# Kernel optimization log

Hardware: AMD Instinct MI355X
Metric: run time of the kernel (lower is better)

Reference implementation:

```python
import jax, jax.numpy as jnp
import numpy as np

N_TREES, DEPTH, INPUT_DIM, N_CLASSES = 15, 3, 128, 10
N_LEAVES = 2 ** DEPTH
N_INTERNAL = N_LEAVES - 1


def _path_masks(depth):
    """Right/left ancestor indicator matrices [n_leaves, n_internal]."""
    n_leaves = 2 ** depth
    n_int = n_leaves - 1
    R = np.zeros((n_leaves, n_int), np.float32)
    L = np.zeros((n_leaves, n_int), np.float32)
    for leaf in range(n_leaves):
        node = leaf + n_int
        for _ in range(depth):
            parent = (node - 1) // 2
            if node % 2 == 0:
                R[leaf, parent] = 1.0
            else:
                L[leaf, parent] = 1.0
            node = parent
    return R, L

_R, _L = _path_masks(DEPTH)


def setup_inputs() -> dict:
    key = jax.random.key(0)
    k1, k2 = jax.random.split(key)
    batch = 262144
    per_tree = N_INTERNAL * INPUT_DIM + N_INTERNAL + N_LEAVES * N_CLASSES
    total = N_TREES * per_tree + N_TREES
    x = jax.random.normal(k1, (batch, INPUT_DIM), dtype=jnp.float32)
    params = jax.random.normal(k2, (total,), dtype=jnp.float32)
    return {"x": x, "params": params}


def reference(x, params):
    per_tree = N_INTERNAL * INPUT_DIM + N_INTERNAL + N_LEAVES * N_CLASSES
    blocks = params[: N_TREES * per_tree].reshape(N_TREES, per_tree)
    w_end = N_INTERNAL * INPUT_DIM
    split_w = blocks[:, :w_end].reshape(N_TREES, N_INTERNAL, INPUT_DIM)
    split_b = blocks[:, w_end : w_end + N_INTERNAL]  # [T, n_internal]
    leaf_logits = blocks[:, w_end + N_INTERNAL :].reshape(N_TREES, N_LEAVES, N_CLASSES)
    tree_w_logits = params[N_TREES * per_tree :]  # [T]

    # split logits z: [B, T, n_internal]
    z = jnp.einsum("bd,tnd->btn", x, split_w) + split_b[None, :, :]
    log_p = jax.nn.log_sigmoid(z)        # log sigma(z)
    log_1mp = jax.nn.log_sigmoid(-z)     # log (1 - sigma(z))

    R = jnp.asarray(_R)
    L = jnp.asarray(_L)
    # path product in log domain: [B, T, n_leaves]
    leaf_probs = jnp.exp(
        jnp.einsum("btn,ln->btl", log_p, R) + jnp.einsum("btn,ln->btl", log_1mp, L)
    )

    leaf_class_probs = jax.nn.softmax(leaf_logits, axis=-1)  # [T, n_leaves, C]
    tree_pred = jnp.einsum("btl,tlc->btc", leaf_probs, leaf_class_probs)
    tree_weights = jax.nn.softmax(tree_w_logits, axis=0)     # [T]
    final_pred = jnp.einsum("btc,t->bc", tree_pred, tree_weights)
    return final_pred
```

## Files before the change

kernel.cpp:

```cpp
#include <hip/hip_runtime.h>
#include <hip/hip_fp16.h>


typedef float    f32x4 __attribute__((ext_vector_type(4)));
typedef _Float16 half8 __attribute__((ext_vector_type(8)));

#define TREES      15
#define IDIM       128
#define NCLS       10
#define NINT       7
#define NLVS       8
#define PER_TREE   (NINT*IDIM + NINT + NLVS*NCLS)
#define NODES      (TREES*NINT)
#define NPAD       112
#define MROWS      128
#define LSTR       136
#define KPAD       128

__global__ __launch_bounds__(256) void prep_kernel(const float* __restrict__ p,
                                                   _Float16* __restrict__ wq,
                                                   float* __restrict__ bq,
                                                   _Float16* __restrict__ wbT) {
    const int gid = blockIdx.x * 256 + threadIdx.x;
    const int nthr = gridDim.x * 256;

    for (int i = gid; i < NPAD * IDIM; i += nthr) {
        int g = i >> 7, k = i & 127;
        float v = 0.f;
        if (g < NODES) {
            int t = g / NINT, n = g % NINT;
            v = p[t * PER_TREE + n * IDIM + k];
        }
        wq[i] = (_Float16)v;
    }
    for (int i = gid; i < NPAD; i += nthr) {
        float v = 0.f;
        if (i < NODES) {
            int t = i / NINT, n = i % NINT;
            v = p[t * PER_TREE + NINT * IDIM + n];
        }
        bq[i] = v;
    }
    const float* tl = p + TREES * PER_TREE;
    for (int i = gid; i < 16 * KPAD; i += nthr) {
        int c = i >> 7, k = i & 127;
        float v = 0.f;
        if (c < NCLS && k < TREES * NLVS) {
            int t = k >> 3, l = k & 7;
            const float* ll = p + t * PER_TREE + NINT * IDIM + NINT + l * NCLS;
            float mx = ll[0];
            #pragma unroll
            for (int j = 1; j < NCLS; ++j) mx = fmaxf(mx, ll[j]);
            float se = 0.f;
            #pragma unroll
            for (int j = 0; j < NCLS; ++j) se += __expf(ll[j] - mx);
            float lsm = __expf(ll[c] - mx) / se;

            float m2 = tl[0];
            #pragma unroll
            for (int j = 1; j < TREES; ++j) m2 = fmaxf(m2, tl[j]);
            float s2 = 0.f;
            #pragma unroll
            for (int j = 0; j < TREES; ++j) s2 += __expf(tl[j] - m2);
            float tw = __expf(tl[t] - m2) / s2;
            v = lsm * tw;
        }
        wbT[i] = (_Float16)v;
    }
}

__global__ __launch_bounds__(256, 4) void tree_main(const float* __restrict__ x,
                                                    const _Float16* __restrict__ wq,
                                                    const float* __restrict__ bq,
                                                    const _Float16* __restrict__ wbT,
                                                    float* __restrict__ out) {
    __shared__ _Float16 s_sh[MROWS * LSTR];

    const int tid  = threadIdx.x;
    const int lane = tid & 63;
    const int wave = tid >> 6;
    const int lm   = lane & 15;
    const int lq   = lane >> 4;

    const int T0 = wave;
    const int T1 = wave + 4;
    const bool two = (T1 < 7);
    half8 bf0[4], bf1[4];
    float bb0 = bq[16 * T0 + lm];
    float bb1 = two ? bq[16 * T1 + lm] : 0.f;
    #pragma unroll
    for (int s = 0; s < 4; ++s)
        bf0[s] = *reinterpret_cast<const half8*>(wq + (16 * T0 + lm) * IDIM + 32 * s + 8 * lq);
    if (two) {
        #pragma unroll
        for (int s = 0; s < 4; ++s)
            bf1[s] = *reinterpret_cast<const half8*>(wq + (16 * T1 + lm) * IDIM + 32 * s + 8 * lq);
    }

    const long base_row = (long)blockIdx.x * MROWS;

    for (int mt = 0; mt < 8; ++mt) {
        const float* xr = x + (base_row + mt * 16 + lm) * IDIM + 8 * lq;
        half8 af[4];
        #pragma unroll
        for (int s = 0; s < 4; ++s) {
            f32x4 f0 = *reinterpret_cast<const f32x4*>(xr + 32 * s);
            f32x4 f1 = *reinterpret_cast<const f32x4*>(xr + 32 * s + 4);
            half8 a;
            #pragma unroll
            for (int j = 0; j < 4; ++j) {
                a[j]     = (_Float16)f0[j];
                a[j + 4] = (_Float16)f1[j];
            }
            af[s] = a;
        }

        f32x4 acc0 = {0.f, 0.f, 0.f, 0.f};
        #pragma unroll
        for (int s = 0; s < 4; ++s)
            acc0 = __builtin_amdgcn_mfma_f32_16x16x32_f16(af[s], bf0[s], acc0, 0, 0, 0);
        {
            const int colbase = 16 * T0 + lm;
            #pragma unroll
            for (int r = 0; r < 4; ++r) {
                float z  = acc0[r] + bb0;
                float sg = __builtin_amdgcn_rcpf(1.0f + __expf(-z));
                s_sh[(mt * 16 + lq * 4 + r) * LSTR + colbase] = (_Float16)sg;
            }
        }
        if (two) {
            f32x4 acc1 = {0.f, 0.f, 0.f, 0.f};
            #pragma unroll
            for (int s = 0; s < 4; ++s)
                acc1 = __builtin_amdgcn_mfma_f32_16x16x32_f16(af[s], bf1[s], acc1, 0, 0, 0);
            const int colbase = 16 * T1 + lm;
            #pragma unroll
            for (int r = 0; r < 4; ++r) {
                float z  = acc1[r] + bb1;
                float sg = __builtin_amdgcn_rcpf(1.0f + __expf(-z));
                s_sh[(mt * 16 + lq * 4 + r) * LSTR + colbase] = (_Float16)sg;
            }
        }
    }
    __syncthreads();

    {
        const int row = tid & 127;
        const int h   = tid >> 7;
        const _Float16* sr = s_sh + row * LSTR + 56 * h;
        half8 sv[8];
        #pragma unroll
        for (int j = 0; j < 8; ++j)
            sv[j] = *reinterpret_cast<const half8*>(sr + 8 * j);

        half8 leafv[8];
        #pragma unroll
        for (int tt = 0; tt < 8; ++tt) {
            if (h == 1 && tt == 7) {
                half8 zz = {(_Float16)0.f, (_Float16)0.f, (_Float16)0.f, (_Float16)0.f,
                            (_Float16)0.f, (_Float16)0.f, (_Float16)0.f, (_Float16)0.f};
                leafv[7] = zz;
            } else {
                float s0 = (float)sv[(7*tt+0) >> 3][(7*tt+0) & 7];
                float s1 = (float)sv[(7*tt+1) >> 3][(7*tt+1) & 7];
                float s2 = (float)sv[(7*tt+2) >> 3][(7*tt+2) & 7];
                float s3 = (float)sv[(7*tt+3) >> 3][(7*tt+3) & 7];
                float s4 = (float)sv[(7*tt+4) >> 3][(7*tt+4) & 7];
                float s5 = (float)sv[(7*tt+5) >> 3][(7*tt+5) & 7];
                float s6 = (float)sv[(7*tt+6) >> 3][(7*tt+6) & 7];
                float u1 = 1.f - s0, u2 = s0;
                float q1 = u1 * s1, q0 = u1 - q1;
                float q3 = u2 * s2, q2 = u2 - q3;
                float L1 = q0 * s3, L0 = q0 - L1;
                float L3 = q1 * s4, L2 = q1 - L3;
                float L5 = q2 * s5, L4 = q2 - L5;
                float L7 = q3 * s6, L6 = q3 - L7;
                half8 lv;
                lv[0] = (_Float16)L0; lv[1] = (_Float16)L1;
                lv[2] = (_Float16)L2; lv[3] = (_Float16)L3;
                lv[4] = (_Float16)L4; lv[5] = (_Float16)L5;
                lv[6] = (_Float16)L6; lv[7] = (_Float16)L7;
                leafv[tt] = lv;
            }
        }
        __syncthreads();
        _Float16* lw = s_sh + row * LSTR + 64 * h;
        #pragma unroll
        for (int j = 0; j < 8; ++j)
            *reinterpret_cast<half8*>(lw + 8 * j) = leafv[j];
    }
    __syncthreads();

    {
        half8 wbf[4];
        #pragma unroll
        for (int s = 0; s < 4; ++s)
            wbf[s] = *reinterpret_cast<const half8*>(wbT + lm * KPAD + 32 * s + 8 * lq);

        #pragma unroll
        for (int u = 0; u < 2; ++u) {
            const int mt = wave + 4 * u;
            half8 af[4];
            #pragma unroll
            for (int s = 0; s < 4; ++s)
                af[s] = *reinterpret_cast<const half8*>(s_sh + (16 * mt + lm) * LSTR + 32 * s + 8 * lq);
            f32x4 acc = {0.f, 0.f, 0.f, 0.f};
            #pragma unroll
            for (int s = 0; s < 4; ++s)
                acc = __builtin_amdgcn_mfma_f32_16x16x32_f16(af[s], wbf[s], acc, 0, 0, 0);
            if (lm < NCLS) {
                #pragma unroll
                for (int r = 0; r < 4; ++r)
                    out[(base_row + 16 * mt + 4 * lq + r) * NCLS + lm] = acc[r];
            }
        }
    }
}

extern "C" void kernel_launch(void* const* d_in, const int* in_sizes, int n_in,
                              void* d_out, int out_size, void* d_ws, size_t ws_size,
                              hipStream_t stream) {
    const float* x      = (const float*)d_in[0];
    const float* params = (const float*)d_in[1];
    float* out = (float*)d_out;

    _Float16* wq  = (_Float16*)d_ws;
    float*    bq  = (float*)((char*)d_ws + NPAD * IDIM * 2);
    _Float16* wbT = (_Float16*)((char*)bq + NPAD * 4);

    const int batch  = in_sizes[0] / IDIM;
    const int blocks = batch / MROWS;

    prep_kernel<<<8, 256, 0, stream>>>(params, wq, bq, wbT);
    tree_main<<<blocks, 256, 0, stream>>>(x, wq, bq, wbT, out);
}
```

Measured before the change: 221.6 us.

## Persistent blocks with double-buffered direct-to-LDS x loads and per-wave row tiles

Replaces the one-block-per-128-rows design with 512 persistent blocks. Each wave owns 16 rows per tile, loads all 7 weight fragments into registers, and prefetches the next tile's x straight into LDS via global_load_lds with a swizzled layout, so the loads overlap with compute. Block-wide barriers go away because each wave reuses its own LDS quarter for the sigmoid, leaf and output stages. This trades higher register use (2 waves/SIMD bound) and a hand-coded waitcnt for latency hiding, and it assumes the batch divides evenly into 512*64 rows.

```diff
diff --git a/kernel.cpp b/kernel.cpp
--- a/kernel.cpp
+++ b/kernel.cpp
@@ -13,15 +13,15 @@
 #define PER_TREE   (NINT*IDIM + NINT + NLVS*NCLS)
 #define NODES      (TREES*NINT)
 #define NPAD       112
-#define MROWS      128
-#define LSTR       136
 #define KPAD       128
+#define RSTR       272
+#define NBLK       512
 
 __global__ __launch_bounds__(256) void prep_kernel(const float* __restrict__ p,
                                                    _Float16* __restrict__ wq,
                                                    float* __restrict__ bq,
                                                    _Float16* __restrict__ wbT) {
-    const int gid = blockIdx.x * 256 + threadIdx.x;
+    const int gid  = blockIdx.x * 256 + threadIdx.x;
     const int nthr = gridDim.x * 256;
 
     for (int i = gid; i < NPAD * IDIM; i += nthr) {
@@ -69,43 +69,69 @@
     }
 }
 
-__global__ __launch_bounds__(256, 4) void tree_main(const float* __restrict__ x,
+__device__ __forceinline__ void dma_quarter(const float* __restrict__ x,
+                                            long grow0, char* qdst, int lane) {
+    const int slot = lane & 31;
+    #pragma unroll
+    for (int it = 0; it < 8; ++it) {
+        int r   = 2 * it + (lane >> 5);
+        int c16 = (slot - r) & 31;
+        const float* gp = x + (grow0 + r) * IDIM + c16 * 4;
+        __builtin_amdgcn_global_load_lds(
+            (const __attribute__((address_space(1))) void*)gp,
+            (__attribute__((address_space(3))) void*)(qdst + it * 1024),
+            16, 0, 0);
+    }
+}
+
+__global__ __launch_bounds__(256, 2) void tree_main(const float* __restrict__ x,
                                                     const _Float16* __restrict__ wq,
                                                     const float* __restrict__ bq,
                                                     const _Float16* __restrict__ wbT,
-                                                    float* __restrict__ out) {
-    __shared__ _Float16 s_sh[MROWS * LSTR];
+                                                    float* __restrict__ out,
+                                                    int tpb) {
+    __shared__ __align__(16) char lds[2][32768];
 
     const int tid  = threadIdx.x;
     const int lane = tid & 63;
-    const int wave = tid >> 6;
+    const int w    = tid >> 6;
     const int lm   = lane & 15;
     const int lq   = lane >> 4;
-
-    const int T0 = wave;
-    const int T1 = wave + 4;
-    const bool two = (T1 < 7);
-    half8 bf0[4], bf1[4];
-    float bb0 = bq[16 * T0 + lm];
-    float bb1 = two ? bq[16 * T1 + lm] : 0.f;
+    const int rg   = lane >> 2;
+    const int g    = lane & 3;
+
+    const long tile0 = (long)blockIdx.x * tpb;
+
+    dma_quarter(x, tile0 * 64 + 16 * w, &lds[0][w * 8192], lane);
+
+    half8 bf[7][4];
+    float bb[7];
+    #pragma unroll
+    for (int nt = 0; nt < 7; ++nt) {
+        bb[nt] = bq[16 * nt + lm];
+        #pragma unroll
+        for (int s = 0; s < 4; ++s)
+            bf[nt][s] = *reinterpret_cast<const half8*>(wq + (16 * nt + lm) * IDIM + 32 * s + 8 * lq);
+    }
+    half8 wbf[4];
     #pragma unroll
     for (int s = 0; s < 4; ++s)
-        bf0[s] = *reinterpret_cast<const half8*>(wq + (16 * T0 + lm) * IDIM + 32 * s + 8 * lq);
-    if (two) {
-        #pragma unroll
-        for (int s = 0; s < 4; ++s)
-            bf1[s] = *reinterpret_cast<const half8*>(wq + (16 * T1 + lm) * IDIM + 32 * s + 8 * lq);
-    }
-
-    const long base_row = (long)blockIdx.x * MROWS;
-
-    for (int mt = 0; mt < 8; ++mt) {
-        const float* xr = x + (base_row + mt * 16 + lm) * IDIM + 8 * lq;
+        wbf[s] = *reinterpret_cast<const half8*>(wbT + lm * KPAD + 32 * s + 8 * lq);
+
+    for (int i = 0; i < tpb; ++i) {
+        char* qcur = &lds[i & 1][w * 8192];
+        const long grow = (tile0 + i) * 64;
+
+        asm volatile("" ::: "memory");
+        __builtin_amdgcn_s_waitcnt(0x0F70);
+        asm volatile("" ::: "memory");
+
         half8 af[4];
         #pragma unroll
         for (int s = 0; s < 4; ++s) {
-            f32x4 f0 = *reinterpret_cast<const f32x4*>(xr + 32 * s);
-            f32x4 f1 = *reinterpret_cast<const f32x4*>(xr + 32 * s + 4);
+            int cc = 8 * s + 2 * lq;
+            f32x4 f0 = *(const f32x4*)(qcur + lm * 512 + (((cc     + lm) & 31) << 4));
+            f32x4 f1 = *(const f32x4*)(qcur + lm * 512 + (((cc + 1 + lm) & 31) << 4));
             half8 a;
             #pragma unroll
             for (int j = 0; j < 4; ++j) {
@@ -115,59 +141,40 @@
             af[s] = a;
         }
 
-        f32x4 acc0 = {0.f, 0.f, 0.f, 0.f};
+        if (i + 1 < tpb)
+            dma_quarter(x, (tile0 + i + 1) * 64 + 16 * w, &lds[(i + 1) & 1][w * 8192], lane);
+
         #pragma unroll
-        for (int s = 0; s < 4; ++s)
-            acc0 = __builtin_amdgcn_mfma_f32_16x16x32_f16(af[s], bf0[s], acc0, 0, 0, 0);
+        for (int nt = 0; nt < 7; ++nt) {
+            f32x4 acc = {0.f, 0.f, 0.f, 0.f};
+            #pragma unroll
+            for (int s = 0; s < 4; ++s)
+                acc = __builtin_amdgcn_mfma_f32_16x16x32_f16(af[s], bf[nt][s], acc, 0, 0, 0);
+            int node = 16 * nt + lm;
+            int col  = node + ((node * 9363) >> 16);
+            #pragma unroll
+            for (int r = 0; r < 4; ++r) {
+                float z  = acc[r] + bb[nt];
+                float sg = __builtin_amdgcn_rcpf(1.0f + __expf(-z));
+                *(_Float16*)(qcur + (4 * lq + r) * RSTR + col * 2) = (_Float16)sg;
+            }
+        }
+
         {
-            const int colbase = 16 * T0 + lm;
-            #pragma unroll
-            for (int r = 0; r < 4; ++r) {
-                float z  = acc0[r] + bb0;
-                float sg = __builtin_amdgcn_rcpf(1.0f + __expf(-z));
-                s_sh[(mt * 16 + lq * 4 + r) * LSTR + colbase] = (_Float16)sg;
-            }
-        }
-        if (two) {
-            f32x4 acc1 = {0.f, 0.f, 0.f, 0.f};
-            #pragma unroll
-            for (int s = 0; s < 4; ++s)
-                acc1 = __builtin_amdgcn_mfma_f32_16x16x32_f16(af[s], bf1[s], acc1, 0, 0, 0);
-            const int colbase = 16 * T1 + lm;
-            #pragma unroll
-            for (int r = 0; r < 4; ++r) {
-                float z  = acc1[r] + bb1;
-                float sg = __builtin_amdgcn_rcpf(1.0f + __expf(-z));
-                s_sh[(mt * 16 + lq * 4 + r) * LSTR + colbase] = (_Float16)sg;
-            }
-        }
-    }
-    __syncthreads();
-
-    {
-        const int row = tid & 127;
-        const int h   = tid >> 7;
-        const _Float16* sr = s_sh + row * LSTR + 56 * h;
-        half8 sv[8];
-        #pragma unroll
-        for (int j = 0; j < 8; ++j)
-            sv[j] = *reinterpret_cast<const half8*>(sr + 8 * j);
-
-        half8 leafv[8];
-        #pragma unroll
-        for (int tt = 0; tt < 8; ++tt) {
-            if (h == 1 && tt == 7) {
-                half8 zz = {(_Float16)0.f, (_Float16)0.f, (_Float16)0.f, (_Float16)0.f,
-                            (_Float16)0.f, (_Float16)0.f, (_Float16)0.f, (_Float16)0.f};
-                leafv[7] = zz;
-            } else {
-                float s0 = (float)sv[(7*tt+0) >> 3][(7*tt+0) & 7];
-                float s1 = (float)sv[(7*tt+1) >> 3][(7*tt+1) & 7];
-                float s2 = (float)sv[(7*tt+2) >> 3][(7*tt+2) & 7];
-                float s3 = (float)sv[(7*tt+3) >> 3][(7*tt+3) & 7];
-                float s4 = (float)sv[(7*tt+4) >> 3][(7*tt+4) & 7];
-                float s5 = (float)sv[(7*tt+5) >> 3][(7*tt+5) & 7];
-                float s6 = (float)sv[(7*tt+6) >> 3][(7*tt+6) & 7];
+            const char* rowp = qcur + rg * RSTR;
+            float sgv[4][7];
+            #pragma unroll
+            for (int tt = 0; tt < 4; ++tt) {
+                int t = 4 * g + tt;
+                #pragma unroll
+                for (int n = 0; n < 7; ++n)
+                    sgv[tt][n] = (float)*(const _Float16*)(rowp + (8 * t + n) * 2);
+            }
+            half8 lv[4];
+            #pragma unroll
+            for (int tt = 0; tt < 4; ++tt) {
+                float s0 = sgv[tt][0], s1 = sgv[tt][1], s2 = sgv[tt][2];
+                float s3 = sgv[tt][3], s4 = sgv[tt][4], s5 = sgv[tt][5], s6 = sgv[tt][6];
                 float u1 = 1.f - s0, u2 = s0;
                 float q1 = u1 * s1, q0 = u1 - q1;
                 float q3 = u2 * s2, q2 = u2 - q3;
@@ -175,43 +182,32 @@
                 float L3 = q1 * s4, L2 = q1 - L3;
                 float L5 = q2 * s5, L4 = q2 - L5;
                 float L7 = q3 * s6, L6 = q3 - L7;
-                half8 lv;
-                lv[0] = (_Float16)L0; lv[1] = (_Float16)L1;
-                lv[2] = (_Float16)L2; lv[3] = (_Float16)L3;
-                lv[4] = (_Float16)L4; lv[5] = (_Float16)L5;
-                lv[6] = (_Float16)L6; lv[7] = (_Float16)L7;
-                leafv[tt] = lv;
-            }
-        }
-        __syncthreads();
-        _Float16* lw = s_sh + row * LSTR + 64 * h;
-        #pragma unroll
-        for (int j = 0; j < 8; ++j)
-            *reinterpret_cast<half8*>(lw + 8 * j) = leafv[j];
-    }
-    __syncthreads();
-
-    {
-        half8 wbf[4];
-        #pragma unroll
-        for (int s = 0; s < 4; ++s)
-            wbf[s] = *reinterpret_cast<const half8*>(wbT + lm * KPAD + 32 * s + 8 * lq);
-
-        #pragma unroll
-        for (int u = 0; u < 2; ++u) {
-            const int mt = wave + 4 * u;
-            half8 af[4];
+                float m = (4 * g + tt < TREES) ? 1.f : 0.f;
+                half8 lv8;
+                lv8[0] = (_Float16)(L0 * m); lv8[1] = (_Float16)(L1 * m);
+                lv8[2] = (_Float16)(L2 * m); lv8[3] = (_Float16)(L3 * m);
+                lv8[4] = (_Float16)(L4 * m); lv8[5] = (_Float16)(L5 * m);
+                lv8[6] = (_Float16)(L6 * m); lv8[7] = (_Float16)(L7 * m);
+                lv[tt] = lv8;
+            }
+            #pragma unroll
+            for (int tt = 0; tt < 4; ++tt)
+                *(half8*)(qcur + rg * RSTR + 64 * g + 16 * tt) = lv[tt];
+        }
+
+        {
+            half8 af2[4];
             #pragma unroll
             for (int s = 0; s < 4; ++s)
-                af[s] = *reinterpret_cast<const half8*>(s_sh + (16 * mt + lm) * LSTR + 32 * s + 8 * lq);
-            f32x4 acc = {0.f, 0.f, 0.f, 0.f};
+                af2[s] = *(const half8*)(qcur + lm * RSTR + 64 * s + 16 * lq);
+            f32x4 a2 = {0.f, 0.f, 0.f, 0.f};
             #pragma unroll
             for (int s = 0; s < 4; ++s)
-                acc = __builtin_amdgcn_mfma_f32_16x16x32_f16(af[s], wbf[s], acc, 0, 0, 0);
+                a2 = __builtin_amdgcn_mfma_f32_16x16x32_f16(af2[s], wbf[s], a2, 0, 0, 0);
             if (lm < NCLS) {
                 #pragma unroll
                 for (int r = 0; r < 4; ++r)
-                    out[(base_row + 16 * mt + 4 * lq + r) * NCLS + lm] = acc[r];
+                    out[(grow + 16 * w + 4 * lq + r) * NCLS + lm] = a2[r];
             }
         }
     }
@@ -228,9 +224,10 @@
     float*    bq  = (float*)((char*)d_ws + NPAD * IDIM * 2);
     _Float16* wbT = (_Float16*)((char*)bq + NPAD * 4);
 
-    const int batch  = in_sizes[0] / IDIM;
-    const int blocks = batch / MROWS;
+    const int batch = in_sizes[0] / IDIM;
+    const int tiles = batch / 64;
+    const int tpb   = tiles / NBLK;
 
     prep_kernel<<<8, 256, 0, stream>>>(params, wq, bq, wbT);
-    tree_main<<<blocks, 256, 0, stream>>>(x, wq, bq, wbT, out);
-}
+    tree_main<<<NBLK, 256, 0, stream>>>(x, wq, bq, wbT, out, tpb);
+}
```

After: 204.3 us. -7.8%, faster.
